# Kernel tuning notes

Hardware: AMD Instinct MI355X
Metric: run time of the kernel (lower is better)

## Reference

```python
import jax, jax.numpy as jnp
import numpy as np

N_NODES = 50000
N_EDGES = 800000
HIDDEN = 128
EDGE_DIM = 16
N_HEADS = 8
HEAD_DIM = HIDDEN // N_HEADS
SCALE = 1.0 / np.sqrt(HEAD_DIM).astype(np.float32)
LN_EPS = 1e-5


def setup_inputs() -> dict:
    key = jax.random.key(0)
    ks = jax.random.split(key, 24)
    s = 0.02

    def w(k, shape):
        return jax.random.normal(k, shape, dtype=jnp.float32) * s

    inp = {
        "node_features": jax.random.normal(ks[0], (N_NODES, HIDDEN), dtype=jnp.float32),
        "edge_index": jax.random.randint(ks[1], (2, N_EDGES), 0, N_NODES, dtype=jnp.int32),
        "edge_features": jax.random.normal(ks[2], (N_EDGES, EDGE_DIM), dtype=jnp.float32),
        # projections stored as [in, out] (y = x @ W + b)
        "Wq": w(ks[3], (HIDDEN, HIDDEN)), "bq": jnp.zeros((HIDDEN,), jnp.float32),
        "Wk": w(ks[4], (HIDDEN, HIDDEN)), "bk": jnp.zeros((HIDDEN,), jnp.float32),
        "Wv": w(ks[5], (HIDDEN, HIDDEN)), "bv": jnp.zeros((HIDDEN,), jnp.float32),
        "Wb1": w(ks[6], (EDGE_DIM, N_HEADS)), "bb1": jnp.zeros((N_HEADS,), jnp.float32),
        "Wb2": w(ks[7], (N_HEADS, N_HEADS)), "bb2": jnp.zeros((N_HEADS,), jnp.float32),
        "Wo": w(ks[8], (HIDDEN, HIDDEN)), "bo": jnp.zeros((HIDDEN,), jnp.float32),
        "Wf1": w(ks[9], (HIDDEN, 2 * HIDDEN)), "bf1": jnp.zeros((2 * HIDDEN,), jnp.float32),
        "Wf2": w(ks[10], (2 * HIDDEN, HIDDEN)), "bf2": jnp.zeros((HIDDEN,), jnp.float32),
        "g1": jnp.ones((HIDDEN,), jnp.float32), "be1": jnp.zeros((HIDDEN,), jnp.float32),
        "g2": jnp.ones((HIDDEN,), jnp.float32), "be2": jnp.zeros((HIDDEN,), jnp.float32),
    }
    return inp


def _layer_norm(x, gamma, beta):
    mu = jnp.mean(x, axis=-1, keepdims=True)
    var = jnp.mean(jnp.square(x - mu), axis=-1, keepdims=True)
    return (x - mu) * jax.lax.rsqrt(var + LN_EPS) * gamma + beta


def reference(node_features, edge_index, edge_features,
              Wq, bq, Wk, bk, Wv, bv, Wb1, bb1, Wb2, bb2,
              Wo, bo, Wf1, bf1, Wf2, bf2, g1, be1, g2, be2):
    n_nodes = node_features.shape[0]
    src, dst = edge_index[0], edge_index[1]

    q = (node_features @ Wq + bq).reshape(n_nodes, N_HEADS, HEAD_DIM)
    k = (node_features @ Wk + bk).reshape(n_nodes, N_HEADS, HEAD_DIM)
    v = (node_features @ Wv + bv).reshape(n_nodes, N_HEADS, HEAD_DIM)

    # per-edge attention logits [E, H]
    edge_bias = jax.nn.silu(edge_features @ Wb1 + bb1) @ Wb2 + bb2
    logits = jnp.sum(q[dst] * k[src], axis=-1) * SCALE + edge_bias

    # segment softmax over edges sharing the same dst node
    max_s = jax.ops.segment_max(logits, dst, num_segments=n_nodes)
    exp_s = jnp.exp(logits - max_s[dst])
    norm = jax.ops.segment_sum(exp_s, dst, num_segments=n_nodes)
    attn = exp_s / jnp.clip(norm[dst], 1e-12)

    # weighted aggregation [N, H, D] -> [N, hidden]
    weighted = attn[:, :, None] * v[src]
    aggregated = jax.ops.segment_sum(weighted, dst, num_segments=n_nodes)
    aggregated = aggregated.reshape(n_nodes, HIDDEN)

    x = _layer_norm(node_features + (aggregated @ Wo + bo), g1, be1)
    ffn = jax.nn.silu(x @ Wf1 + bf1) @ Wf2 + bf2
    return _layer_norm(x + ffn, g2, be2)
```

## Files before the change

### kernel.cpp

```cpp
#include <hip/hip_runtime.h>
#include <hip/hip_bf16.h>
#include <math.h>

#define HIDDEN 128
#define EDGE_DIM 16
#define N_HEADS 8
#define QK_SCALE 0.25f
#define LN_EPS 1e-5f

using bf16x8 = __attribute__((ext_vector_type(8))) short;
using f32x4 = __attribute__((ext_vector_type(4))) float;
using f32x4v = __attribute__((ext_vector_type(4))) float;
typedef __hip_bfloat16 bf16;

__device__ __forceinline__ float b2f(short u) {
  union { unsigned int i; float f; } c;
  c.i = ((unsigned int)(unsigned short)u) << 16;
  return c.f;
}
__device__ __forceinline__ short f2b(float f) {
  bf16 h = __float2bfloat16(f);
  union { bf16 b; short s; } c;
  c.b = h;
  return c.s;
}

__global__ __launch_bounds__(256) void conv_weights_kernel(
    const float* __restrict__ Wq, const float* __restrict__ Wk, const float* __restrict__ Wv,
    const float* __restrict__ bq, const float* __restrict__ bk, const float* __restrict__ bv,
    const float* __restrict__ Wo, const float* __restrict__ Wf1, const float* __restrict__ Wf2,
    bf16* __restrict__ Wqkv_t, bf16* __restrict__ Wo_t, bf16* __restrict__ Wf1_t,
    bf16* __restrict__ Wf2_t, float* __restrict__ bqkv) {
  int i = blockIdx.x * 256 + threadIdx.x;
  if (i < 49152) {
    int n = i >> 7, k = i & 127;
    const float* W = (n < 128) ? Wq : ((n < 256) ? Wk : Wv);
    int nn = n & 127;
    Wqkv_t[i] = __float2bfloat16(W[k * 128 + nn]);
  } else if (i < 65536) {
    int j = i - 49152;
    int n = j >> 7, k = j & 127;
    Wo_t[j] = __float2bfloat16(Wo[k * 128 + n]);
  } else if (i < 98304) {
    int j = i - 65536;
    int n = j >> 7, k = j & 127;
    Wf1_t[j] = __float2bfloat16(Wf1[k * 256 + n]);
  } else if (i < 131072) {
    int j = i - 98304;
    int n = j >> 8, k = j & 255;
    Wf2_t[j] = __float2bfloat16(Wf2[k * 128 + n]);
  }
  if (i < 384) bqkv[i] = (i < 128) ? bq[i] : ((i < 256) ? bk[i - 128] : bv[i - 256]);
}

template <int K, int EPI, int OUTBF, int AF32>
__global__ __launch_bounds__(256) void mfma_gemm_kernel(
    const void* __restrict__ Ap, const bf16* __restrict__ Wt,
    const float* __restrict__ bias, void* __restrict__ Cout, int M, int Nc) {
  const int tid = threadIdx.x;
  const int w = tid >> 6, l = tid & 63;
  const int wr = w >> 1, wc = w & 1;
  const int lr = l & 15, lk = l >> 4;
  const int bm = blockIdx.y * 64;
  const int bn = blockIdx.x * 128 + wc * 64;

  f32x4 acc[2][4] = {};
  const int arow0 = bm + wr * 32 + lr;

  for (int k0 = 0; k0 < K; k0 += 128) {
    bf16x8 bfr[4][4];
#pragma unroll
    for (int fn = 0; fn < 4; ++fn) {
      const bf16* wp = Wt + (size_t)(bn + fn * 16 + lr) * K + k0 + lk * 8;
#pragma unroll
      for (int ks = 0; ks < 4; ++ks) bfr[fn][ks] = *(const bf16x8*)(wp + ks * 32);
    }
    bf16x8 afr[2][4];
#pragma unroll
    for (int fr = 0; fr < 2; ++fr) {
      int row = arow0 + fr * 16;
      if (row >= M) row = M - 1;
      if (AF32) {
        const float* ap = (const float*)Ap + (size_t)row * K + k0 + lk * 8;
#pragma unroll
        for (int ks = 0; ks < 4; ++ks) {
          float4 x = *(const float4*)(ap + ks * 32);
          float4 y = *(const float4*)(ap + ks * 32 + 4);
          bf16x8 t;
          t[0] = f2b(x.x); t[1] = f2b(x.y); t[2] = f2b(x.z); t[3] = f2b(x.w);
          t[4] = f2b(y.x); t[5] = f2b(y.y); t[6] = f2b(y.z); t[7] = f2b(y.w);
          afr[fr][ks] = t;
        }
      } else {
        const bf16* ap = (const bf16*)Ap + (size_t)row * K + k0 + lk * 8;
#pragma unroll
        for (int ks = 0; ks < 4; ++ks) afr[fr][ks] = *(const bf16x8*)(ap + ks * 32);
      }
    }
#pragma unroll
    for (int ks = 0; ks < 4; ++ks)
#pragma unroll
      for (int fr = 0; fr < 2; ++fr)
#pragma unroll
        for (int fn = 0; fn < 4; ++fn)
          acc[fr][fn] = __builtin_amdgcn_mfma_f32_16x16x32_bf16(afr[fr][ks], bfr[fn][ks],
                                                                acc[fr][fn], 0, 0, 0);
  }

#pragma unroll
  for (int fn = 0; fn < 4; ++fn) {
    const int col = bn + fn * 16 + lr;
    const float bv = bias[col];
#pragma unroll
    for (int fr = 0; fr < 2; ++fr) {
      const int rbase = bm + wr * 32 + fr * 16 + lk * 4;
#pragma unroll
      for (int r = 0; r < 4; ++r) {
        int row = rbase + r;
        if (row < M) {
          float o = acc[fr][fn][r] + bv;
          if (EPI == 1) o = o / (1.f + __expf(-o));
          if (OUTBF)
            ((bf16*)Cout)[(size_t)row * Nc + col] = __float2bfloat16(o);
          else
            ((float*)Cout)[(size_t)row * Nc + col] = o;
        }
      }
    }
  }
}

template <int K>
__global__ __launch_bounds__(256) void mfma_gemm_ln_kernel(
    const bf16* __restrict__ A, const bf16* __restrict__ Wt,
    const float* __restrict__ bias, const float* __restrict__ R,
    const float* __restrict__ gam, const float* __restrict__ bet,
    float* __restrict__ y, bf16* __restrict__ yb, int M) {
  const int tid = threadIdx.x;
  const int w = tid >> 6, l = tid & 63;
  const int wr = w >> 1, wc = w & 1;
  const int lr = l & 15, lk = l >> 4;
  const int bm = blockIdx.x * 64;
  const int bn = wc * 64;

  f32x4 acc[2][4] = {};
  const int arow0 = bm + wr * 32 + lr;

  for (int k0 = 0; k0 < K; k0 += 128) {
    bf16x8 bfr[4][4];
#pragma unroll
    for (int fn = 0; fn < 4; ++fn) {
      const bf16* wp = Wt + (size_t)(bn + fn * 16 + lr) * K + k0 + lk * 8;
#pragma unroll
      for (int ks = 0; ks < 4; ++ks) bfr[fn][ks] = *(const bf16x8*)(wp + ks * 32);
    }
    bf16x8 afr[2][4];
#pragma unroll
    for (int fr = 0; fr < 2; ++fr) {
      int row = arow0 + fr * 16;
      if (row >= M) row = M - 1;
      const bf16* ap = A + (size_t)row * K + k0 + lk * 8;
#pragma unroll
      for (int ks = 0; ks < 4; ++ks) afr[fr][ks] = *(const bf16x8*)(ap + ks * 32);
    }
#pragma unroll
    for (int ks = 0; ks < 4; ++ks)
#pragma unroll
      for (int fr = 0; fr < 2; ++fr)
#pragma unroll
        for (int fn = 0; fn < 4; ++fn)
          acc[fr][fn] = __builtin_amdgcn_mfma_f32_16x16x32_bf16(afr[fr][ks], bfr[fn][ks],
                                                                acc[fr][fn], 0, 0, 0);
  }

  float bv[4], gv[4], ev[4];
#pragma unroll
  for (int fn = 0; fn < 4; ++fn) {
    int col = bn + fn * 16 + lr;
    bv[fn] = bias[col];
    gv[fn] = gam[col];
    ev[fn] = bet[col];
  }
  float ps[2][4], psq[2][4];
#pragma unroll
  for (int fr = 0; fr < 2; ++fr) {
#pragma unroll
    for (int r = 0; r < 4; ++r) {
      int row = bm + wr * 32 + fr * 16 + lk * 4 + r;
      int rrow = (row < M) ? row : (M - 1);
      float s = 0.f, sq = 0.f;
#pragma unroll
      for (int fn = 0; fn < 4; ++fn) {
        int col = bn + fn * 16 + lr;
        float o = acc[fr][fn][r] + bv[fn] + R[(size_t)rrow * HIDDEN + col];
        acc[fr][fn][r] = o;
        s += o;
        sq += o * o;
      }
      ps[fr][r] = s;
      psq[fr][r] = sq;
    }
  }
#pragma unroll
  for (int off = 1; off < 16; off <<= 1) {
#pragma unroll
    for (int fr = 0; fr < 2; ++fr)
#pragma unroll
      for (int r = 0; r < 4; ++r) {
        ps[fr][r] += __shfl_xor(ps[fr][r], off, 64);
        psq[fr][r] += __shfl_xor(psq[fr][r], off, 64);
      }
  }
  __shared__ float s_sum[2][64], s_sq[2][64];
  if (lr == 0) {
#pragma unroll
    for (int fr = 0; fr < 2; ++fr)
#pragma unroll
      for (int r = 0; r < 4; ++r) {
        int rl = wr * 32 + fr * 16 + lk * 4 + r;
        s_sum[wc][rl] = ps[fr][r];
        s_sq[wc][rl] = psq[fr][r];
      }
  }
  __syncthreads();
#pragma unroll
  for (int fr = 0; fr < 2; ++fr) {
#pragma unroll
    for (int r = 0; r < 4; ++r) {
      int rl = wr * 32 + fr * 16 + lk * 4 + r;
      int row = bm + rl;
      float tot = s_sum[0][rl] + s_sum[1][rl];
      float tsq = s_sq[0][rl] + s_sq[1][rl];
      float mean = tot * (1.f / 128.f);
      float var = tsq * (1.f / 128.f) - mean * mean;
      float rstd = rsqrtf(var + LN_EPS);
      if (row < M) {
#pragma unroll
        for (int fn = 0; fn < 4; ++fn) {
          int col = bn + fn * 16 + lr;
          float val = (acc[fr][fn][r] - mean) * rstd * gv[fn] + ev[fn];
          if (y) y[(size_t)row * HIDDEN + col] = val;
          if (yb) yb[(size_t)row * HIDDEN + col] = __float2bfloat16(val);
        }
      }
    }
  }
}

__global__ void hist_kernel(const int* __restrict__ dst, int* __restrict__ counts, int E) {
  int e = blockIdx.x * blockDim.x + threadIdx.x;
  if (e < E) atomicAdd(&counts[dst[e]], 1);
}

__device__ __forceinline__ int wave_incl_scan(int x, int lane) {
  int incl = x;
#pragma unroll
  for (int off = 1; off < 64; off <<= 1) {
    int y = __shfl_up(incl, off, 64);
    if (lane >= off) incl += y;
  }
  return incl;
}

__global__ __launch_bounds__(256) void scan_block_kernel(const int* __restrict__ counts,
                                                         int* __restrict__ offs,
                                                         int* __restrict__ btot, int N) {
  __shared__ int s4[4];
  int tid = threadIdx.x;
  int i = blockIdx.x * 256 + tid;
  int lane = tid & 63, wv = tid >> 6;
  int x = (i < N) ? counts[i] : 0;
  int incl = wave_incl_scan(x, lane);
  if (lane == 63) s4[wv] = incl;
  __syncthreads();
  if (tid == 0) {
    int s = 0;
#pragma unroll
    for (int j = 0; j < 4; ++j) { int t = s4[j]; s4[j] = s; s += t; }
    btot[blockIdx.x] = s;
  }
  __syncthreads();
  if (i < N) offs[i] = s4[wv] + incl - x;
}

__global__ __launch_bounds__(256) void scan_tot_kernel(int* __restrict__ btot, int nb) {
  __shared__ int s4[4];
  __shared__ int carry;
  int tid = threadIdx.x;
  int lane = tid & 63, wv = tid >> 6;
  if (tid == 0) carry = 0;
  __syncthreads();
  for (int c0 = 0; c0 < nb; c0 += 256) {
    int i = c0 + tid;
    int x = (i < nb) ? btot[i] : 0;
    int incl = wave_incl_scan(x, lane);
    if (lane == 63) s4[wv] = incl;
    __syncthreads();
    if (tid == 0) {
      int s = 0;
#pragma unroll
      for (int j = 0; j < 4; ++j) { int t = s4[j]; s4[j] = s; s += t; }
    }
    __syncthreads();
    int base = carry + s4[wv];
    if (i < nb) btot[i] = base + incl - x;
    __syncthreads();
    if (tid == 255) carry = base + incl;
    __syncthreads();
  }
}

__global__ __launch_bounds__(256) void scan_add_kernel(int* __restrict__ offs,
                                                       const int* __restrict__ btot,
                                                       int N, int E) {
  int i = blockIdx.x * 256 + threadIdx.x;
  if (i < N) offs[i] += btot[blockIdx.x];
  if (i == 0) offs[N] = E;
}

__global__ __launch_bounds__(256) void scatter_mlp_kernel(
    const int* __restrict__ dst, const int* __restrict__ src,
    const float* __restrict__ ef, const float* __restrict__ Wb1,
    const float* __restrict__ bb1, const float* __restrict__ Wb2,
    const float* __restrict__ bb2, const int* __restrict__ offs,
    int* __restrict__ cursor, int2* __restrict__ es_csr,
    bf16* __restrict__ eb, int E) {
  __shared__ float w1[128], w2[64], b1[8], b2[8];
  int tid = threadIdx.x;
  if (tid < 128) w1[tid] = Wb1[tid];
  else if (tid < 192) w2[tid - 128] = Wb2[tid - 128];
  else if (tid < 200) b1[tid - 192] = bb1[tid - 192];
  else if (tid < 208) b2[tid - 200] = bb2[tid - 200];
  __syncthreads();

  int e = blockIdx.x * 256 + tid;
  if (e >= E) return;

  const f32x4v* p4 = (const f32x4v*)(ef + (size_t)e * 16);
  f32x4v f0 = __builtin_nontemporal_load(p4 + 0);
  f32x4v f1 = __builtin_nontemporal_load(p4 + 1);
  f32x4v f2 = __builtin_nontemporal_load(p4 + 2);
  f32x4v f3 = __builtin_nontemporal_load(p4 + 3);
  float x[16] = {f0[0], f0[1], f0[2], f0[3], f1[0], f1[1], f1[2], f1[3],
                 f2[0], f2[1], f2[2], f2[3], f3[0], f3[1], f3[2], f3[3]};

  float h[8];
#pragma unroll
  for (int j = 0; j < 8; ++j) h[j] = b1[j];
#pragma unroll
  for (int i = 0; i < 16; ++i) {
    float xi = x[i];
#pragma unroll
    for (int j = 0; j < 8; ++j) h[j] = fmaf(xi, w1[i * 8 + j], h[j]);
  }
#pragma unroll
  for (int j = 0; j < 8; ++j) h[j] = h[j] / (1.f + __expf(-h[j]));

  float o[8];
#pragma unroll
  for (int j = 0; j < 8; ++j) o[j] = b2[j];
#pragma unroll
  for (int jj = 0; jj < 8; ++jj) {
    float hj = h[jj];
#pragma unroll
    for (int j = 0; j < 8; ++j) o[j] = fmaf(hj, w2[jj * 8 + j], o[j]);
  }
  bf16x8 o8;
#pragma unroll
  for (int j = 0; j < 8; ++j) o8[j] = f2b(o[j]);
  __builtin_nontemporal_store(o8, (bf16x8*)(eb + (size_t)e * 8));

  int d = dst[e];
  int p = offs[d] + atomicAdd(&cursor[d], 1);
  es_csr[p] = make_int2(src[e], e);
}

__global__ __launch_bounds__(256) void node_attn_kernel(
    const bf16* __restrict__ qkv, const int2* __restrict__ es_csr,
    const bf16* __restrict__ eb, const int* __restrict__ offs,
    bf16* __restrict__ agg, int Nn) {
  int n = blockIdx.x * 4 + (threadIdx.x >> 6);
  if (n >= Nn) return;
  int l = threadIdx.x & 63;
  int g = l >> 3;
  int il = l & 7;

  const bf16* qrow = qkv + (size_t)n * 384 + il * 16;
  bf16x8 qa = *(const bf16x8*)(qrow);
  bf16x8 qb = *(const bf16x8*)(qrow + 8);
  float qf[16];
#pragma unroll
  for (int j = 0; j < 8; ++j) {
    qf[j] = b2f(qa[j]) * QK_SCALE;
    qf[8 + j] = b2f(qb[j]) * QK_SCALE;
  }

  int s0 = offs[n], s1 = offs[n + 1];
  float lsum = 0.f;
  float acc[16] = {};

  for (int p0 = s0; p0 < s1; p0 += 8) {
    int p = p0 + g;
    bool valid = p < s1;
    int pc = valid ? p : s1 - 1;
    int2 es = es_csr[pc];
    const bf16* kvrow = qkv + (size_t)es.x * 384 + 128 + il * 16;
    bf16x8 k0 = *(const bf16x8*)(kvrow);
    bf16x8 k1 = *(const bf16x8*)(kvrow + 8);
    bf16x8 v0 = *(const bf16x8*)(kvrow + 128);
    bf16x8 v1 = *(const bf16x8*)(kvrow + 136);
    float ebv = b2f(eb[(size_t)es.y * 8 + il]);

    float prod = 0.f;
#pragma unroll
    for (int j = 0; j < 8; ++j) {
      prod = fmaf(qf[j], b2f(k0[j]), prod);
      prod = fmaf(qf[8 + j], b2f(k1[j]), prod);
    }
    float pe = valid ? __expf(prod + ebv) : 0.f;
    lsum += pe;
#pragma unroll
    for (int j = 0; j < 8; ++j) {
      acc[j] = fmaf(pe, b2f(v0[j]), acc[j]);
      acc[8 + j] = fmaf(pe, b2f(v1[j]), acc[8 + j]);
    }
  }

#pragma unroll
  for (int off = 8; off < 64; off <<= 1) {
    lsum += __shfl_xor(lsum, off, 64);
#pragma unroll
    for (int j = 0; j < 16; ++j) acc[j] += __shfl_xor(acc[j], off, 64);
  }

  if (g == 0) {
    float inv = (lsum > 0.f) ? 1.f / lsum : 0.f;
    bf16x8 o0, o1;
#pragma unroll
    for (int j = 0; j < 8; ++j) {
      o0[j] = f2b(acc[j] * inv);
      o1[j] = f2b(acc[8 + j] * inv);
    }
    bf16* orow = agg + (size_t)n * HIDDEN + il * 16;
    *(bf16x8*)(orow) = o0;
    *(bf16x8*)(orow + 8) = o1;
  }
}

extern "C" void kernel_launch(void* const* d_in, const int* in_sizes, int n_in,
                              void* d_out, int out_size, void* d_ws, size_t ws_size,
                              hipStream_t stream) {
  const float* nf = (const float*)d_in[0];
  const int* ei = (const int*)d_in[1];
  const float* ef = (const float*)d_in[2];
  const float* Wq = (const float*)d_in[3];
  const float* bq = (const float*)d_in[4];
  const float* Wk = (const float*)d_in[5];
  const float* bk_ = (const float*)d_in[6];
  const float* Wv = (const float*)d_in[7];
  const float* bv = (const float*)d_in[8];
  const float* Wb1 = (const float*)d_in[9];
  const float* bb1 = (const float*)d_in[10];
  const float* Wb2 = (const float*)d_in[11];
  const float* bb2 = (const float*)d_in[12];
  const float* Wo = (const float*)d_in[13];
  const float* bo = (const float*)d_in[14];
  const float* Wf1 = (const float*)d_in[15];
  const float* bf1 = (const float*)d_in[16];
  const float* Wf2 = (const float*)d_in[17];
  const float* bf2 = (const float*)d_in[18];
  const float* g1 = (const float*)d_in[19];
  const float* be1 = (const float*)d_in[20];
  const float* g2 = (const float*)d_in[21];
  const float* be2 = (const float*)d_in[22];

  const int N = in_sizes[0] / HIDDEN;
  const int E = in_sizes[2] / EDGE_DIM;
  const int* srcA = ei;
  const int* dstA = ei + E;

  char* base = (char*)d_ws;
  size_t off = 0;
  auto alloc = [&](size_t bytes) {
    off = (off + 255) & ~(size_t)255;
    char* p = base + off;
    off += bytes;
    return p;
  };

  bf16* qkv = (bf16*)alloc((size_t)N * 384 * 2);
  bf16* hbuf = qkv;
  bf16* agg = (bf16*)alloc((size_t)N * HIDDEN * 2);
  float* x1 = (float*)alloc((size_t)N * HIDDEN * 4);
  bf16* x1b = (bf16*)alloc((size_t)N * HIDDEN * 2);
  int2* es_csr = (int2*)alloc((size_t)E * 8);
  bf16* eb = (bf16*)alloc((size_t)E * N_HEADS * 2);
  int* counts = (int*)alloc((size_t)N * 8);
  int* cursor = counts + N;
  int* offs = (int*)alloc((size_t)(N + 1) * 4);
  const int nb = (N + 255) / 256;
  int* btot = (int*)alloc((size_t)nb * 4);
  bf16* Wqkv_t = (bf16*)alloc(384 * 128 * 2);
  bf16* Wo_t = (bf16*)alloc(128 * 128 * 2);
  bf16* Wf1_t = (bf16*)alloc(256 * 128 * 2);
  bf16* Wf2_t = (bf16*)alloc(128 * 256 * 2);
  float* bqkv = (float*)alloc(384 * 4);

  float* outp = (float*)d_out;
  const int mb64 = (N + 63) / 64;
  const int eblocks = (E + 255) / 256;

  conv_weights_kernel<<<512, 256, 0, stream>>>(Wq, Wk, Wv, bq, bk_, bv, Wo, Wf1, Wf2,
                                               Wqkv_t, Wo_t, Wf1_t, Wf2_t, bqkv);

  mfma_gemm_kernel<128, 0, 1, 1><<<dim3(3, mb64), 256, 0, stream>>>(
      nf, Wqkv_t, bqkv, qkv, N, 384);

  hipMemsetAsync(counts, 0, (size_t)N * 8, stream);
  hist_kernel<<<eblocks, 256, 0, stream>>>(dstA, counts, E);
  scan_block_kernel<<<nb, 256, 0, stream>>>(counts, offs, btot, N);
  scan_tot_kernel<<<1, 256, 0, stream>>>(btot, nb);
  scan_add_kernel<<<nb, 256, 0, stream>>>(offs, btot, N, E);
  scatter_mlp_kernel<<<eblocks, 256, 0, stream>>>(dstA, srcA, ef, Wb1, bb1, Wb2, bb2,
                                                  offs, cursor, es_csr, eb, E);

  node_attn_kernel<<<(N + 3) / 4, 256, 0, stream>>>(qkv, es_csr, eb, offs, agg, N);

  mfma_gemm_ln_kernel<128><<<mb64, 256, 0, stream>>>(agg, Wo_t, bo, nf, g1, be1, x1, x1b, N);

  mfma_gemm_kernel<128, 1, 1, 0><<<dim3(2, mb64), 256, 0, stream>>>(
      x1b, Wf1_t, bf1, hbuf, N, 256);

  mfma_gemm_ln_kernel<256><<<mb64, 256, 0, stream>>>(hbuf, Wf2_t, bf2, x1, g2, be2,
                                                     outp, nullptr, N);
}
```

Measured before the change: 308.1 us.

## Store K/V in FP8 and prefetch edge indices in node attention

The QKV projection now writes Q as bf16 and K/V as FP8 into a separate buffer. This halves the bytes each edge gathers for K and V rows in the attention kernel. The CSR array now holds only edge ids, and src is looked up from edge_index with a one-iteration software prefetch. Nodes with no incoming edges exit early. FP8 storage of K/V reduces accuracy and could push the error past tolerance. The extra indirection through srcA adds a dependent load.

```diff
diff --git a/kernel.cpp b/kernel.cpp
--- a/kernel.cpp
+++ b/kernel.cpp
@@ -11,6 +11,8 @@
 using bf16x8 = __attribute__((ext_vector_type(8))) short;
 using f32x4 = __attribute__((ext_vector_type(4))) float;
 using f32x4v = __attribute__((ext_vector_type(4))) float;
+using f32x2 = __attribute__((ext_vector_type(2))) float;
+using i32x4 = __attribute__((ext_vector_type(4))) int;
 typedef __hip_bfloat16 bf16;
 
 __device__ __forceinline__ float b2f(short u) {
@@ -23,6 +25,10 @@
   union { bf16 b; short s; } c;
   c.b = h;
   return c.s;
+}
+__device__ __forceinline__ unsigned char f2fp8(float f) {
+  int pk = __builtin_amdgcn_cvt_pk_fp8_f32(f, f, 0, false);
+  return (unsigned char)(pk & 0xff);
 }
 
 __global__ __launch_bounds__(256) void conv_weights_kernel(
@@ -130,6 +136,77 @@
   }
 }
 
+__global__ __launch_bounds__(256) void mfma_gemm_qkv_kernel(
+    const float* __restrict__ A, const bf16* __restrict__ Wt,
+    const float* __restrict__ bias, bf16* __restrict__ qb,
+    unsigned char* __restrict__ kv8, int M) {
+  const int tid = threadIdx.x;
+  const int w = tid >> 6, l = tid & 63;
+  const int wr = w >> 1, wc = w & 1;
+  const int lr = l & 15, lk = l >> 4;
+  const int bm = blockIdx.y * 64;
+  const int bn = blockIdx.x * 128 + wc * 64;
+
+  f32x4 acc[2][4] = {};
+  const int arow0 = bm + wr * 32 + lr;
+
+  {
+    bf16x8 bfr[4][4];
+#pragma unroll
+    for (int fn = 0; fn < 4; ++fn) {
+      const bf16* wp = Wt + (size_t)(bn + fn * 16 + lr) * 128 + lk * 8;
+#pragma unroll
+      for (int ks = 0; ks < 4; ++ks) bfr[fn][ks] = *(const bf16x8*)(wp + ks * 32);
+    }
+    bf16x8 afr[2][4];
+#pragma unroll
+    for (int fr = 0; fr < 2; ++fr) {
+      int row = arow0 + fr * 16;
+      if (row >= M) row = M - 1;
+      const float* ap = A + (size_t)row * 128 + lk * 8;
+#pragma unroll
+      for (int ks = 0; ks < 4; ++ks) {
+        float4 x = *(const float4*)(ap + ks * 32);
+        float4 y = *(const float4*)(ap + ks * 32 + 4);
+        bf16x8 t;
+        t[0] = f2b(x.x); t[1] = f2b(x.y); t[2] = f2b(x.z); t[3] = f2b(x.w);
+        t[4] = f2b(y.x); t[5] = f2b(y.y); t[6] = f2b(y.z); t[7] = f2b(y.w);
+        afr[fr][ks] = t;
+      }
+    }
+#pragma unroll
+    for (int ks = 0; ks < 4; ++ks)
+#pragma unroll
+      for (int fr = 0; fr < 2; ++fr)
+#pragma unroll
+        for (int fn = 0; fn < 4; ++fn)
+          acc[fr][fn] = __builtin_amdgcn_mfma_f32_16x16x32_bf16(afr[fr][ks], bfr[fn][ks],
+                                                                acc[fr][fn], 0, 0, 0);
+  }
+
+  const bool isQ = (blockIdx.x == 0);
+#pragma unroll
+  for (int fn = 0; fn < 4; ++fn) {
+    const int col = bn + fn * 16 + lr;
+    const float bv = bias[col];
+#pragma unroll
+    for (int fr = 0; fr < 2; ++fr) {
+      const int rbase = bm + wr * 32 + fr * 16 + lk * 4;
+#pragma unroll
+      for (int r = 0; r < 4; ++r) {
+        int row = rbase + r;
+        if (row < M) {
+          float o = acc[fr][fn][r] + bv;
+          if (isQ)
+            qb[(size_t)row * 128 + col] = __float2bfloat16(o);
+          else
+            kv8[(size_t)row * 256 + (col - 128)] = f2fp8(o);
+        }
+      }
+    }
+  }
+}
+
 template <int K>
 __global__ __launch_bounds__(256) void mfma_gemm_ln_kernel(
     const bf16* __restrict__ A, const bf16* __restrict__ Wt,
@@ -319,12 +396,11 @@
 }
 
 __global__ __launch_bounds__(256) void scatter_mlp_kernel(
-    const int* __restrict__ dst, const int* __restrict__ src,
-    const float* __restrict__ ef, const float* __restrict__ Wb1,
-    const float* __restrict__ bb1, const float* __restrict__ Wb2,
-    const float* __restrict__ bb2, const int* __restrict__ offs,
-    int* __restrict__ cursor, int2* __restrict__ es_csr,
-    bf16* __restrict__ eb, int E) {
+    const int* __restrict__ dst, const float* __restrict__ ef,
+    const float* __restrict__ Wb1, const float* __restrict__ bb1,
+    const float* __restrict__ Wb2, const float* __restrict__ bb2,
+    const int* __restrict__ offs, int* __restrict__ cursor,
+    int* __restrict__ eid_csr, bf16* __restrict__ eb, int E) {
   __shared__ float w1[128], w2[64], b1[8], b2[8];
   int tid = threadIdx.x;
   if (tid < 128) w1[tid] = Wb1[tid];
@@ -372,11 +448,12 @@
 
   int d = dst[e];
   int p = offs[d] + atomicAdd(&cursor[d], 1);
-  es_csr[p] = make_int2(src[e], e);
+  __builtin_nontemporal_store(e, eid_csr + p);
 }
 
 __global__ __launch_bounds__(256) void node_attn_kernel(
-    const bf16* __restrict__ qkv, const int2* __restrict__ es_csr,
+    const bf16* __restrict__ qb, const unsigned char* __restrict__ kv8,
+    const int* __restrict__ eid_csr, const int* __restrict__ srcA,
     const bf16* __restrict__ eb, const int* __restrict__ offs,
     bf16* __restrict__ agg, int Nn) {
   int n = blockIdx.x * 4 + (threadIdx.x >> 6);
@@ -385,44 +462,68 @@
   int g = l >> 3;
   int il = l & 7;
 
-  const bf16* qrow = qkv + (size_t)n * 384 + il * 16;
+  int s0 = offs[n], s1 = offs[n + 1];
+  bf16* orow = agg + (size_t)n * HIDDEN + il * 16;
+  if (s0 >= s1) {
+    if (g == 0) {
+      bf16x8 z = {};
+      *(bf16x8*)(orow) = z;
+      *(bf16x8*)(orow + 8) = z;
+    }
+    return;
+  }
+
+  const bf16* qrow = qb + (size_t)n * 128 + il * 16;
   bf16x8 qa = *(const bf16x8*)(qrow);
-  bf16x8 qb = *(const bf16x8*)(qrow + 8);
+  bf16x8 qb8 = *(const bf16x8*)(qrow + 8);
   float qf[16];
 #pragma unroll
   for (int j = 0; j < 8; ++j) {
     qf[j] = b2f(qa[j]) * QK_SCALE;
-    qf[8 + j] = b2f(qb[j]) * QK_SCALE;
-  }
-
-  int s0 = offs[n], s1 = offs[n + 1];
+    qf[8 + j] = b2f(qb8[j]) * QK_SCALE;
+  }
+
   float lsum = 0.f;
   float acc[16] = {};
 
+  int p = s0 + g;
+  int pc = (p < s1) ? p : s1 - 1;
+  int eid = eid_csr[pc];
+  int s = srcA[eid];
+
   for (int p0 = s0; p0 < s1; p0 += 8) {
-    int p = p0 + g;
-    bool valid = p < s1;
-    int pc = valid ? p : s1 - 1;
-    int2 es = es_csr[pc];
-    const bf16* kvrow = qkv + (size_t)es.x * 384 + 128 + il * 16;
-    bf16x8 k0 = *(const bf16x8*)(kvrow);
-    bf16x8 k1 = *(const bf16x8*)(kvrow + 8);
-    bf16x8 v0 = *(const bf16x8*)(kvrow + 128);
-    bf16x8 v1 = *(const bf16x8*)(kvrow + 136);
-    float ebv = b2f(eb[(size_t)es.y * 8 + il]);
+    bool valid = (p0 + g) < s1;
+    int ce = eid, cs = s;
+    int pn = p0 + 8 + g;
+    if (pn < s1) {
+      eid = eid_csr[pn];
+      s = srcA[eid];
+    }
+    float ebv = b2f(eb[(size_t)ce * 8 + il]);
+    const unsigned char* kvrow = kv8 + (size_t)cs * 256 + il * 16;
+    i32x4 kw = *(const i32x4*)(kvrow);
+    i32x4 vw = *(const i32x4*)(kvrow + 128);
 
     float prod = 0.f;
 #pragma unroll
-    for (int j = 0; j < 8; ++j) {
-      prod = fmaf(qf[j], b2f(k0[j]), prod);
-      prod = fmaf(qf[8 + j], b2f(k1[j]), prod);
+    for (int w2 = 0; w2 < 4; ++w2) {
+      f32x2 lo = __builtin_amdgcn_cvt_pk_f32_fp8(kw[w2], false);
+      f32x2 hi = __builtin_amdgcn_cvt_pk_f32_fp8(kw[w2], true);
+      prod = fmaf(qf[w2 * 4 + 0], lo[0], prod);
+      prod = fmaf(qf[w2 * 4 + 1], lo[1], prod);
+      prod = fmaf(qf[w2 * 4 + 2], hi[0], prod);
+      prod = fmaf(qf[w2 * 4 + 3], hi[1], prod);
     }
     float pe = valid ? __expf(prod + ebv) : 0.f;
     lsum += pe;
 #pragma unroll
-    for (int j = 0; j < 8; ++j) {
-      acc[j] = fmaf(pe, b2f(v0[j]), acc[j]);
-      acc[8 + j] = fmaf(pe, b2f(v1[j]), acc[8 + j]);
+    for (int w2 = 0; w2 < 4; ++w2) {
+      f32x2 lo = __builtin_amdgcn_cvt_pk_f32_fp8(vw[w2], false);
+      f32x2 hi = __builtin_amdgcn_cvt_pk_f32_fp8(vw[w2], true);
+      acc[w2 * 4 + 0] = fmaf(pe, lo[0], acc[w2 * 4 + 0]);
+      acc[w2 * 4 + 1] = fmaf(pe, lo[1], acc[w2 * 4 + 1]);
+      acc[w2 * 4 + 2] = fmaf(pe, hi[0], acc[w2 * 4 + 2]);
+      acc[w2 * 4 + 3] = fmaf(pe, hi[1], acc[w2 * 4 + 3]);
     }
   }
 
@@ -441,7 +542,6 @@
       o0[j] = f2b(acc[j] * inv);
       o1[j] = f2b(acc[8 + j] * inv);
     }
-    bf16* orow = agg + (size_t)n * HIDDEN + il * 16;
     *(bf16x8*)(orow) = o0;
     *(bf16x8*)(orow + 8) = o1;
   }
@@ -488,12 +588,17 @@
     return p;
   };
 
-  bf16* qkv = (bf16*)alloc((size_t)N * 384 * 2);
-  bf16* hbuf = qkv;
+  size_t qb_bytes = (size_t)N * 128 * 2;
+  size_t kv_bytes = (size_t)N * 256;
+  size_t hb_bytes = (size_t)N * 256 * 2;
+  char* regB = alloc(hb_bytes > qb_bytes + kv_bytes ? hb_bytes : qb_bytes + kv_bytes);
+  bf16* qb = (bf16*)regB;
+  unsigned char* kv8 = (unsigned char*)(regB + qb_bytes);
+  bf16* hbuf = (bf16*)regB;
   bf16* agg = (bf16*)alloc((size_t)N * HIDDEN * 2);
   float* x1 = (float*)alloc((size_t)N * HIDDEN * 4);
   bf16* x1b = (bf16*)alloc((size_t)N * HIDDEN * 2);
-  int2* es_csr = (int2*)alloc((size_t)E * 8);
+  int* eid_csr = (int*)alloc((size_t)E * 4);
   bf16* eb = (bf16*)alloc((size_t)E * N_HEADS * 2);
   int* counts = (int*)alloc((size_t)N * 8);
   int* cursor = counts + N;
@@ -513,18 +618,18 @@
   conv_weights_kernel<<<512, 256, 0, stream>>>(Wq, Wk, Wv, bq, bk_, bv, Wo, Wf1, Wf2,
                                                Wqkv_t, Wo_t, Wf1_t, Wf2_t, bqkv);
 
-  mfma_gemm_kernel<128, 0, 1, 1><<<dim3(3, mb64), 256, 0, stream>>>(
-      nf, Wqkv_t, bqkv, qkv, N, 384);
+  mfma_gemm_qkv_kernel<<<dim3(3, mb64), 256, 0, stream>>>(nf, Wqkv_t, bqkv, qb, kv8, N);
 
   hipMemsetAsync(counts, 0, (size_t)N * 8, stream);
   hist_kernel<<<eblocks, 256, 0, stream>>>(dstA, counts, E);
   scan_block_kernel<<<nb, 256, 0, stream>>>(counts, offs, btot, N);
   scan_tot_kernel<<<1, 256, 0, stream>>>(btot, nb);
   scan_add_kernel<<<nb, 256, 0, stream>>>(offs, btot, N, E);
-  scatter_mlp_kernel<<<eblocks, 256, 0, stream>>>(dstA, srcA, ef, Wb1, bb1, Wb2, bb2,
-                                                  offs, cursor, es_csr, eb, E);
-
-  node_attn_kernel<<<(N + 3) / 4, 256, 0, stream>>>(qkv, es_csr, eb, offs, agg, N);
+  scatter_mlp_kernel<<<eblocks, 256, 0, stream>>>(dstA, ef, Wb1, bb1, Wb2, bb2,
+                                                  offs, cursor, eid_csr, eb, E);
+
+  node_attn_kernel<<<(N + 3) / 4, 256, 0, stream>>>(qb, kv8, eid_csr, srcA, eb, offs,
+                                                    agg, N);
 
   mfma_gemm_ln_kernel<128><<<mb64, 256, 0, stream>>>(agg, Wo_t, bo, nf, g1, be1, x1, x1b, N);
 
```

Measured after the change: 292.1 us. -5.2%, faster.
